# Kernel tuning notes

Hardware: AMD Instinct MI355X
Metric: run time of the kernel (lower is better)

Reference implementation:

```python
import jax, jax.numpy as jnp
import numpy as np

B, QH, QW = 16, 64, 64
KH, KW = 64, 64
H, D, DK, K, S = 8, 256, 32, 4, 1


def setup_inputs() -> dict:
    key = jax.random.key(0)
    ks = jax.random.split(key, 16)
    def lin(i, din, dout, wscale=1.0):
        w = jax.random.normal(ks[i], (din, dout), jnp.float32) * (wscale / np.sqrt(din))
        b = jax.random.normal(ks[i + 1], (dout,), jnp.float32) * 0.02
        return w, b
    Wq, bq = lin(0, D, D)
    Wb, bb = lin(2, D, D)
    Wk, bk = lin(4, D, D)
    Woff, boff = lin(6, D, 2 * H * K * S, wscale=0.1)  # small offsets keep samples near ref point
    WA, bA = lin(8, D, H * K * S)
    Wm, bm = lin(10, D, D)
    return dict(
        query=jax.random.normal(ks[12], (B, QH, QW, D), jnp.float32),
        keys=jax.random.normal(ks[13], (B, KH, KW, D), jnp.float32),
        ref_point=jax.random.uniform(ks[14], (B, QH, QW, 2), jnp.float32),
        src_query=jax.random.normal(ks[15], (B, QH, QW, D), jnp.float32),
        Wq=Wq, bq=bq, Wb=Wb, bb=bb, Wk=Wk, bk=bk,
        Woff=Woff, boff=boff, WA=WA, bA=bA, Wm=Wm, bm=bm)


def _bilinear_zeros(img, px, py):
    # img [N, Hs, Ws, C]; px, py pixel coords [N, K, QH, QW]
    # Matches torch F.grid_sample(mode='bilinear', padding_mode='zeros'):
    # each out-of-bounds corner contributes zero.
    N, Hs, Ws, _ = img.shape
    x0 = jnp.floor(px); y0 = jnp.floor(py)
    wx1 = px - x0; wy1 = py - y0
    n = jnp.arange(N)[:, None, None, None]
    def corner(xf, yf, w):
        xi = xf.astype(jnp.int32); yi = yf.astype(jnp.int32)
        valid = (xi >= 0) & (xi < Ws) & (yi >= 0) & (yi < Hs)
        v = img[n, jnp.clip(yi, 0, Hs - 1), jnp.clip(xi, 0, Ws - 1)]
        return v * (w * valid)[..., None]
    return (corner(x0, y0, (1 - wx1) * (1 - wy1)) + corner(x0 + 1, y0, wx1 * (1 - wy1))
            + corner(x0, y0 + 1, (1 - wx1) * wy1) + corner(x0 + 1, y0 + 1, wx1 * wy1))


def reference(query, keys, ref_point, src_query, Wq, bq, Wb, bb, Wk, bk,
              Woff, boff, WA, bA, Wm, bm):
    _ = query @ Wq + bq  # q_proj output is computed but unused in the original forward
    sq = src_query @ Wb + bb
    off = (sq @ Woff + boff).reshape(B, QH, QW, H, S, K, 2)
    off = off.transpose(0, 3, 4, 5, 1, 2, 6).reshape(B * H, S, K, QH, QW, 2)
    A = jax.nn.softmax((sq @ WA + bA).reshape(B, QH, QW, H, S * K), axis=-1)
    A = A.transpose(0, 3, 1, 2, 4).reshape(B * H, QH, QW, S, K)
    # k_proj on the (single-scale) key feature map -> per-head maps [B*H, KH, KW, DK]
    kf = (keys @ Wk + bk).reshape(B, KH, KW, H, DK).transpose(0, 3, 1, 2, 4).reshape(B * H, KH, KW, DK)
    # restore_scale then torch .repeat(h,1,1,1): flat index n -> batch n % B (faithful to original)
    rr = ref_point * jnp.array([KW - 1, KH - 1], jnp.float32)
    rr = jnp.tile(rr, (H, 1, 1, 1))  # [B*H, QH, QW, 2]
    samples = []
    for l in range(S):
        pts = rr[:, None] + off[:, l]                 # [B*H, K, QH, QW, 2]
        vgx = 2.0 * pts[..., 0] / max(KW - 1, 1) - 1.0
        vgy = 2.0 * pts[..., 1] / max(KH - 1, 1) - 1.0
        px = ((vgx + 1.0) * KW - 1.0) / 2.0           # grid_sample align_corners=False unnormalize
        py = ((vgy + 1.0) * KH - 1.0) / 2.0
        samples.append(_bilinear_zeros(kf, px, py))   # [B*H, K, QH, QW, DK]
    samp = jnp.stack(samples, axis=1)                 # [B*H, S, K, QH, QW, DK]
    feat = jnp.einsum('nskhwd,nhwsk->nhwd', samp, A)  # weighted sum over scales*points
    feat = feat.reshape(B, H, QH, QW, DK).transpose(0, 2, 3, 1, 4).reshape(B, QH, QW, D)
    return feat @ Wm + bm
```

## Files before the change

kernel.cpp:

```cpp
#include <hip/hip_runtime.h>
#include <hip/hip_bf16.h>

using bf16 = __hip_bfloat16;
typedef short bf16x8 __attribute__((ext_vector_type(8)));
typedef float f32x4 __attribute__((ext_vector_type(4)));

#define DD 256
#define MTOT 65536

static __device__ __forceinline__ short f2bs(float f) {
    bf16 h = __float2bfloat16(f);
    return *reinterpret_cast<short*>(&h);
}
static __device__ __forceinline__ float bs2f(short s) {
    unsigned u = (unsigned)(unsigned short)s << 16;
    return __uint_as_float(u);
}

static __device__ __forceinline__ void gll16(const void* g, void* l) {
    __builtin_amdgcn_global_load_lds(
        (const __attribute__((address_space(1))) unsigned int*)g,
        (__attribute__((address_space(3))) unsigned int*)l, 16, 0, 0);
}

static __device__ __forceinline__ int swz_idx(int n, int k) {
    return n * 256 + ((((k >> 3) ^ (n & 7)) << 3) | (k & 7));
}

__global__ __launch_bounds__(256) void k_transpose(
    const float* __restrict__ Wb, const float* __restrict__ Wk, const float* __restrict__ Wm,
    const float* __restrict__ Woff, const float* __restrict__ WA,
    bf16* __restrict__ WbT, bf16* __restrict__ WkT, bf16* __restrict__ WmT,
    bf16* __restrict__ WoffAT)
{
    int idx = blockIdx.x * 256 + threadIdx.x;
    if (idx < 3 * 65536) {
        int which = idx >> 16, e = idx & 65535;
        int i = e >> 8, j = e & 255;
        const float* src = which == 0 ? Wb : (which == 1 ? Wk : Wm);
        bf16*        dst = which == 0 ? WbT : (which == 1 ? WkT : WmT);
        dst[swz_idx(j, i)] = __float2bfloat16(src[e]);
    } else {
        int e = idx - 3 * 65536;
        if (e < 96 * 256) {
            int j = e >> 8, i = e & 255;
            WoffAT[swz_idx(j, i)] = __float2bfloat16((j < 64) ? Woff[i * 64 + j]
                                                              : WA[i * 32 + (j - 64)]);
        }
    }
}

template <int NTW, int NCOLS, bool AF32>
static __device__ __forceinline__ void gemm_lds2(
    const void* __restrict__ Av, const bf16* __restrict__ BTswz,
    bf16* __restrict__ Bs, char* __restrict__ As,
    int row0, int tid, f32x4 (&acc)[2][NTW])
{
    const int wave = tid >> 6, lane = tid & 63;
    const int rg = wave >> 1, cg = wave & 1;
    const int rsub = lane & 15, kg = lane >> 4;
    constexpr int SB = NCOLS / 32;
    constexpr int SA = AF32 ? 4 : 2;
    constexpr int ABYTES = AF32 ? 16384 : 8192;

    auto stageB = [&](int s) {
#pragma unroll
        for (int i = 0; i < SB; ++i) {
            int cc = wave * SB + i;
            int i16 = cc * 64 + lane;
            int n = i16 >> 3, lg = i16 & 7;
            gll16(BTswz + (size_t)n * 256 + s * 64 + lg * 8, (char*)Bs + (size_t)i16 * 16);
        }
    };
    auto stageA = [&](int s, int buf) {
#pragma unroll
        for (int i = 0; i < SA; ++i) {
            if constexpr (AF32) {
                int cc = wave * 4 + i;
                int row = cc * 4 + (lane >> 4);
                int g = (lane & 15) ^ (row & 15);
                gll16((const float*)Av + (size_t)(row0 + row) * DD + s * 64 + g * 4,
                      As + (size_t)buf * ABYTES + cc * 1024 + lane * 16);
            } else {
                int cc = wave * 2 + i;
                int row = cc * 8 + (lane >> 3);
                int g = (lane & 7) ^ (row & 7);
                gll16((const bf16*)Av + (size_t)(row0 + row) * DD + s * 64 + g * 8,
                      As + (size_t)buf * ABYTES + cc * 1024 + lane * 16);
            }
        }
    };

    stageA(0, 0);
    int cur = 0;
#pragma unroll
    for (int s = 0; s < 4; ++s) {
        stageB(s);
        if (s < 3) {
            stageA(s + 1, cur ^ 1);
            asm volatile("s_waitcnt vmcnt(%0)" :: "i"(SA) : "memory");
        } else {
            asm volatile("s_waitcnt vmcnt(0)" ::: "memory");
        }
        __builtin_amdgcn_s_barrier();
#pragma unroll
        for (int kkl = 0; kkl < 2; ++kkl) {
            bf16x8 afr[2];
#pragma unroll
            for (int st = 0; st < 2; ++st) {
                int row = rg * 32 + st * 16 + rsub;
                if constexpr (AF32) {
                    const char* base = As + cur * ABYTES + row * 256;
                    int G0 = kkl * 8 + kg * 2;
                    f32x4 v0 = *(const f32x4*)(base + ((G0 ^ (row & 15)) << 4));
                    f32x4 v1 = *(const f32x4*)(base + (((G0 + 1) ^ (row & 15)) << 4));
                    bf16x8 a;
#pragma unroll
                    for (int e = 0; e < 4; ++e) { a[e] = f2bs(v0[e]); a[e + 4] = f2bs(v1[e]); }
                    afr[st] = a;
                } else {
                    const char* base = As + cur * ABYTES + row * 128;
                    int g = kkl * 4 + kg;
                    afr[st] = *(const bf16x8*)(base + ((g ^ (row & 7)) << 4));
                }
            }
            int lg = kkl * 4 + kg;
#pragma unroll
            for (int nt = 0; nt < NTW; ++nt) {
                int n = cg * (NTW * 16) + nt * 16 + rsub;
                bf16x8 b = *(const bf16x8*)((const char*)Bs + (size_t)n * 128 + ((lg ^ (n & 7)) << 4));
                acc[0][nt] = __builtin_amdgcn_mfma_f32_16x16x32_bf16(afr[0], b, acc[0][nt], 0, 0, 0);
                acc[1][nt] = __builtin_amdgcn_mfma_f32_16x16x32_bf16(afr[1], b, acc[1][nt], 0, 0, 0);
            }
        }
        asm volatile("s_waitcnt lgkmcnt(0)" ::: "memory");
        __builtin_amdgcn_s_barrier();
        cur ^= 1;
    }
}

__global__ __launch_bounds__(256) void k_gemm_sq(
    const float* __restrict__ src, const bf16* __restrict__ WbT,
    const float* __restrict__ bb, bf16* __restrict__ sq)
{
    __shared__ __align__(16) bf16 Bs[256 * 64];
    __shared__ __align__(16) char As[2 * 16384];
    int tid = threadIdx.x, lane = tid & 63, wave = tid >> 6;
    int row0 = blockIdx.x * 64;
    f32x4 acc[2][8] = {};
    gemm_lds2<8, 256, true>(src, WbT, Bs, As, row0, tid, acc);
    int col = lane & 15;
    int jbase = (wave & 1) * 128;
    int rb = row0 + (wave >> 1) * 32 + ((lane >> 4) << 2);
#pragma unroll
    for (int mt = 0; mt < 2; ++mt)
#pragma unroll
        for (int nt = 0; nt < 8; ++nt) {
            int j = jbase + nt * 16 + col;
            float bias = bb[j];
#pragma unroll
            for (int r = 0; r < 4; ++r)
                sq[(size_t)(rb + mt * 16 + r) * DD + j] =
                    __float2bfloat16(acc[mt][nt][r] + bias);
        }
}

__global__ __launch_bounds__(256) void k_gemm_offA(
    const bf16* __restrict__ sq, const bf16* __restrict__ WoffAT,
    const float* __restrict__ boff, const float* __restrict__ bA,
    float* __restrict__ off_ws, float* __restrict__ A_ws)
{
    __shared__ __align__(16) bf16 Bs[96 * 64];
    __shared__ __align__(16) char As[2 * 8192];
    int tid = threadIdx.x, lane = tid & 63, wave = tid >> 6;
    int row0 = blockIdx.x * 64;
    f32x4 acc[2][3] = {};
    gemm_lds2<3, 96, false>(sq, WoffAT, Bs, As, row0, tid, acc);
    int col = lane & 15;
    int jbase = (wave & 1) * 48;
    int rb = row0 + (wave >> 1) * 32 + ((lane >> 4) << 2);
#pragma unroll
    for (int mt = 0; mt < 2; ++mt) {
#pragma unroll
        for (int nt = 0; nt < 3; ++nt) {
            int j = jbase + nt * 16 + col;
            if (j < 64) {
                float bias = boff[j];
#pragma unroll
                for (int r = 0; r < 4; ++r) {
                    int m = rb + mt * 16 + r;
                    off_ws[(size_t)m * 64 + j] = acc[mt][nt][r] + bias;
                }
            } else {
                int ac = j - 64;
                float bias = bA[ac];
#pragma unroll
                for (int r = 0; r < 4; ++r) {
                    int m = rb + mt * 16 + r;
                    float v  = acc[mt][nt][r] + bias;
                    float mx = fmaxf(v, __shfl_xor(v, 1));
                    mx       = fmaxf(mx, __shfl_xor(mx, 2));
                    float e  = __expf(v - mx);
                    float su = e + __shfl_xor(e, 1);
                    su      += __shfl_xor(su, 2);
                    A_ws[(size_t)m * 32 + ac] = e / su;
                }
            }
        }
    }
}

__global__ __launch_bounds__(256) void k_gemm_kf(
    const float* __restrict__ keys, const bf16* __restrict__ WkT,
    const float* __restrict__ bk, bf16* __restrict__ kf)
{
    __shared__ __align__(16) bf16 Bs[256 * 64];
    __shared__ __align__(16) char As[2 * 16384];
    int tid = threadIdx.x, lane = tid & 63, wave = tid >> 6;
    int row0 = blockIdx.x * 64;
    f32x4 acc[2][8] = {};
    gemm_lds2<8, 256, true>(keys, WkT, Bs, As, row0, tid, acc);
    int col = lane & 15;
    int jbase = (wave & 1) * 128;
    int rb = row0 + (wave >> 1) * 32 + ((lane >> 4) << 2);
#pragma unroll
    for (int mt = 0; mt < 2; ++mt)
#pragma unroll
        for (int nt = 0; nt < 8; ++nt) {
            int j = jbase + nt * 16 + col;
            float bias = bk[j];
#pragma unroll
            for (int r = 0; r < 4; ++r) {
                int m = rb + mt * 16 + r;
                size_t dst = (((size_t)(m >> 12) * 8 + (j >> 5)) * 4096 + (m & 4095)) * 32 + (j & 31);
                kf[dst] = __float2bfloat16(acc[mt][nt][r] + bias);
            }
        }
}

__global__ __launch_bounds__(256) void k_sample(
    const float* __restrict__ ref_point, const float* __restrict__ off_ws,
    const float* __restrict__ A_ws, const bf16* __restrict__ kf,
    bf16* __restrict__ feat)
{
    int t  = threadIdx.x;
    int q  = t >> 5;
    int h  = (t >> 2) & 7;
    int cg = t & 3;
    int m  = blockIdx.x * 8 + q;
    int b  = m >> 12, pix = m & 4095;
    int rbatch = (b * 8 + h) & 15;
    const float* rp = ref_point + ((size_t)rbatch * 4096 + pix) * 2;
    float rx = rp[0] * 63.0f;
    float ry = rp[1] * 63.0f;
    const bf16* kfh = kf + ((size_t)(b * 8 + h) * 4096) * 32 + cg * 8;
    float acc[8] = {};
#pragma unroll
    for (int k = 0; k < 4; ++k) {
        const float* op = off_ws + (size_t)m * 64 + (h * 4 + k) * 2;
        float ox = op[0], oy = op[1];
        float a  = A_ws[(size_t)m * 32 + h * 4 + k];
        float px = (rx + ox) * (64.0f / 63.0f) - 0.5f;
        float py = (ry + oy) * (64.0f / 63.0f) - 0.5f;
        float x0 = floorf(px), y0 = floorf(py);
        float wx1 = px - x0, wy1 = py - y0;
        int xi = (int)x0, yi = (int)y0;
        float ax0 = (1.f - wx1) * ((xi     >= 0 && xi     < 64) ? 1.f : 0.f);
        float ax1 = wx1         * ((xi + 1 >= 0 && xi + 1 < 64) ? 1.f : 0.f);
        float ay0 = (1.f - wy1) * ((yi     >= 0 && yi     < 64) ? a : 0.f);
        float ay1 = wy1         * ((yi + 1 >= 0 && yi + 1 < 64) ? a : 0.f);
        int xc0 = min(max(xi, 0), 63),      xc1 = min(max(xi + 1, 0), 63);
        int yc0 = min(max(yi, 0), 63) * 64, yc1 = min(max(yi + 1, 0), 63) * 64;
        bf16x8 v00 = *(const bf16x8*)(kfh + (yc0 + xc0) * 32);
        bf16x8 v01 = *(const bf16x8*)(kfh + (yc0 + xc1) * 32);
        bf16x8 v10 = *(const bf16x8*)(kfh + (yc1 + xc0) * 32);
        bf16x8 v11 = *(const bf16x8*)(kfh + (yc1 + xc1) * 32);
        float w00 = ax0 * ay0, w01 = ax1 * ay0, w10 = ax0 * ay1, w11 = ax1 * ay1;
#pragma unroll
        for (int e = 0; e < 8; ++e) {
            acc[e] += w00 * bs2f(v00[e]) + w01 * bs2f(v01[e])
                    + w10 * bs2f(v10[e]) + w11 * bs2f(v11[e]);
        }
    }
    bf16x8 o;
#pragma unroll
    for (int e = 0; e < 8; ++e) o[e] = f2bs(acc[e]);
    *(bf16x8*)(feat + (size_t)m * DD + h * 32 + cg * 8) = o;
}

__global__ __launch_bounds__(256) void k_gemm_out(
    const bf16* __restrict__ feat, const bf16* __restrict__ WmT,
    const float* __restrict__ bm, float* __restrict__ out)
{
    __shared__ __align__(16) bf16 Bs[256 * 64];
    __shared__ __align__(16) char As[2 * 8192];
    int tid = threadIdx.x, lane = tid & 63, wave = tid >> 6;
    int row0 = blockIdx.x * 64;
    f32x4 acc[2][8] = {};
    gemm_lds2<8, 256, false>(feat, WmT, Bs, As, row0, tid, acc);
    int col = lane & 15;
    int jbase = (wave & 1) * 128;
    int rb = row0 + (wave >> 1) * 32 + ((lane >> 4) << 2);
#pragma unroll
    for (int mt = 0; mt < 2; ++mt)
#pragma unroll
        for (int nt = 0; nt < 8; ++nt) {
            int j = jbase + nt * 16 + col;
            float bias = bm[j];
#pragma unroll
            for (int r = 0; r < 4; ++r)
                out[(size_t)(rb + mt * 16 + r) * DD + j] =
                    acc[mt][nt][r] + bias;
        }
}

extern "C" void kernel_launch(void* const* d_in, const int* in_sizes, int n_in,
                              void* d_out, int out_size, void* d_ws, size_t ws_size,
                              hipStream_t stream)
{
    (void)in_sizes; (void)n_in; (void)out_size; (void)ws_size;
    const float* keys = (const float*)d_in[1];
    const float* refp = (const float*)d_in[2];
    const float* srcq = (const float*)d_in[3];
    const float* Wb   = (const float*)d_in[6];
    const float* bb   = (const float*)d_in[7];
    const float* Wk   = (const float*)d_in[8];
    const float* bk   = (const float*)d_in[9];
    const float* Woff = (const float*)d_in[10];
    const float* boff = (const float*)d_in[11];
    const float* WA   = (const float*)d_in[12];
    const float* bA   = (const float*)d_in[13];
    const float* Wm   = (const float*)d_in[14];
    const float* bm   = (const float*)d_in[15];

    char* ws = (char*)d_ws;
    bf16*  WbT    = (bf16*)(ws + 0);
    bf16*  WkT    = (bf16*)(ws + 131072);
    bf16*  WmT    = (bf16*)(ws + 262144);
    bf16*  WoffAT = (bf16*)(ws + 393216);
    bf16*  sq_ws  = (bf16*)(ws + 442368);
    bf16*  kf_ws  = (bf16*)(ws + 442368 + 33554432ull);
    bf16*  feat_ws= (bf16*)(ws + 442368 + 2ull * 33554432ull);
    float* off_ws = (float*)(ws + 442368 + 3ull * 33554432ull);
    float* A_ws   = (float*)(ws + 442368 + 3ull * 33554432ull + 16777216ull);

    float* out = (float*)d_out;

    k_transpose<<<864, 256, 0, stream>>>(Wb, Wk, Wm, Woff, WA, WbT, WkT, WmT, WoffAT);
    k_gemm_sq  <<<1024, 256, 0, stream>>>(srcq, WbT, bb, sq_ws);
    k_gemm_kf  <<<1024, 256, 0, stream>>>(keys, WkT, bk, kf_ws);
    k_gemm_offA<<<1024, 256, 0, stream>>>(sq_ws, WoffAT, boff, bA, off_ws, A_ws);
    k_sample   <<<8192, 256, 0, stream>>>(refp, off_ws, A_ws, kf_ws, feat_ws);
    k_gemm_out <<<1024, 256, 0, stream>>>(feat_ws, WmT, bm, out);
}
```

Before: 134.7 us.

## Fuse sq projection with offset/attention GEMM via LDS and remap sample blocks by XCD

```diff
diff --git a/kernel.cpp b/kernel.cpp
--- a/kernel.cpp
+++ b/kernel.cpp
@@ -139,9 +139,10 @@
     }
 }
 
-__global__ __launch_bounds__(256) void k_gemm_sq(
-    const float* __restrict__ src, const bf16* __restrict__ WbT,
-    const float* __restrict__ bb, bf16* __restrict__ sq)
+__global__ __launch_bounds__(256) void k_gemm_sqoffA(
+    const float* __restrict__ src, const bf16* __restrict__ WbT, const float* __restrict__ bb,
+    const bf16* __restrict__ WoffAT, const float* __restrict__ boff, const float* __restrict__ bA,
+    float* __restrict__ off_ws, float* __restrict__ A_ws)
 {
     __shared__ __align__(16) bf16 Bs[256 * 64];
     __shared__ __align__(16) char As[2 * 16384];
@@ -149,36 +150,77 @@
     int row0 = blockIdx.x * 64;
     f32x4 acc[2][8] = {};
     gemm_lds2<8, 256, true>(src, WbT, Bs, As, row0, tid, acc);
+
+    {
+        int col = lane & 15;
+        int jbase = (wave & 1) * 128;
+        int lrb = (wave >> 1) * 32 + ((lane >> 4) << 2);
+#pragma unroll
+        for (int mt = 0; mt < 2; ++mt)
+#pragma unroll
+            for (int nt = 0; nt < 8; ++nt) {
+                int j = jbase + nt * 16 + col;
+                float bias = bb[j];
+                int g = j >> 3;
+#pragma unroll
+                for (int r = 0; r < 4; ++r) {
+                    int lr = lrb + mt * 16 + r;
+                    *(short*)(As + lr * 512 + (((g ^ (lr & 7)) << 4)) + (j & 7) * 2) =
+                        f2bs(acc[mt][nt][r] + bias);
+                }
+            }
+    }
+    __syncthreads();
+
+    f32x4 acc2[2][3] = {};
+    const int rsub = lane & 15, kg = lane >> 4;
+    const int rg = wave >> 1, cg2 = wave & 1;
+    auto stageOB = [&](int s, int buf) {
+#pragma unroll
+        for (int i = 0; i < 3; ++i) {
+            int i16 = (wave * 3 + i) * 64 + lane;
+            int n = i16 >> 3, lg = i16 & 7;
+            gll16(WoffAT + (size_t)n * 256 + s * 64 + lg * 8,
+                  (char*)Bs + buf * 12288 + (size_t)i16 * 16);
+        }
+    };
+    stageOB(0, 0);
+    int cur = 0;
+#pragma unroll
+    for (int s = 0; s < 4; ++s) {
+        if (s < 3) {
+            stageOB(s + 1, cur ^ 1);
+            asm volatile("s_waitcnt vmcnt(3)" ::: "memory");
+        } else {
+            asm volatile("s_waitcnt vmcnt(0)" ::: "memory");
+        }
+        __builtin_amdgcn_s_barrier();
+#pragma unroll
+        for (int kkl = 0; kkl < 2; ++kkl) {
+            bf16x8 afr[2];
+#pragma unroll
+            for (int st = 0; st < 2; ++st) {
+                int lr = rg * 32 + st * 16 + rsub;
+                int g = s * 8 + kkl * 4 + kg;
+                afr[st] = *(const bf16x8*)(As + lr * 512 + ((g ^ (lr & 7)) << 4));
+            }
+            int lg = kkl * 4 + kg;
+#pragma unroll
+            for (int nt = 0; nt < 3; ++nt) {
+                int n = cg2 * 48 + nt * 16 + rsub;
+                bf16x8 b = *(const bf16x8*)((const char*)Bs + cur * 12288 + (size_t)n * 128
+                                            + ((lg ^ (n & 7)) << 4));
+                acc2[0][nt] = __builtin_amdgcn_mfma_f32_16x16x32_bf16(afr[0], b, acc2[0][nt], 0, 0, 0);
+                acc2[1][nt] = __builtin_amdgcn_mfma_f32_16x16x32_bf16(afr[1], b, acc2[1][nt], 0, 0, 0);
+            }
+        }
+        asm volatile("s_waitcnt lgkmcnt(0)" ::: "memory");
+        __builtin_amdgcn_s_barrier();
+        cur ^= 1;
+    }
     int col = lane & 15;
-    int jbase = (wave & 1) * 128;
-    int rb = row0 + (wave >> 1) * 32 + ((lane >> 4) << 2);
-#pragma unroll
-    for (int mt = 0; mt < 2; ++mt)
-#pragma unroll
-        for (int nt = 0; nt < 8; ++nt) {
-            int j = jbase + nt * 16 + col;
-            float bias = bb[j];
-#pragma unroll
-            for (int r = 0; r < 4; ++r)
-                sq[(size_t)(rb + mt * 16 + r) * DD + j] =
-                    __float2bfloat16(acc[mt][nt][r] + bias);
-        }
-}
-
-__global__ __launch_bounds__(256) void k_gemm_offA(
-    const bf16* __restrict__ sq, const bf16* __restrict__ WoffAT,
-    const float* __restrict__ boff, const float* __restrict__ bA,
-    float* __restrict__ off_ws, float* __restrict__ A_ws)
-{
-    __shared__ __align__(16) bf16 Bs[96 * 64];
-    __shared__ __align__(16) char As[2 * 8192];
-    int tid = threadIdx.x, lane = tid & 63, wave = tid >> 6;
-    int row0 = blockIdx.x * 64;
-    f32x4 acc[2][3] = {};
-    gemm_lds2<3, 96, false>(sq, WoffAT, Bs, As, row0, tid, acc);
-    int col = lane & 15;
-    int jbase = (wave & 1) * 48;
-    int rb = row0 + (wave >> 1) * 32 + ((lane >> 4) << 2);
+    int jbase = cg2 * 48;
+    int rb = row0 + rg * 32 + ((lane >> 4) << 2);
 #pragma unroll
     for (int mt = 0; mt < 2; ++mt) {
 #pragma unroll
@@ -189,7 +231,7 @@
 #pragma unroll
                 for (int r = 0; r < 4; ++r) {
                     int m = rb + mt * 16 + r;
-                    off_ws[(size_t)m * 64 + j] = acc[mt][nt][r] + bias;
+                    off_ws[(size_t)m * 64 + j] = acc2[mt][nt][r] + bias;
                 }
             } else {
                 int ac = j - 64;
@@ -197,7 +239,7 @@
 #pragma unroll
                 for (int r = 0; r < 4; ++r) {
                     int m = rb + mt * 16 + r;
-                    float v  = acc[mt][nt][r] + bias;
+                    float v  = acc2[mt][nt][r] + bias;
                     float mx = fmaxf(v, __shfl_xor(v, 1));
                     mx       = fmaxf(mx, __shfl_xor(mx, 2));
                     float e  = __expf(v - mx);
@@ -243,12 +285,16 @@
     const float* __restrict__ A_ws, const bf16* __restrict__ kf,
     bf16* __restrict__ feat)
 {
+    int bid = blockIdx.x;
+    int xcd = bid & 7, within = bid >> 3;
+    int bb_ = xcd * 2 + (within >> 9);
+    int pixblk = within & 511;
     int t  = threadIdx.x;
     int q  = t >> 5;
     int h  = (t >> 2) & 7;
     int cg = t & 3;
-    int m  = blockIdx.x * 8 + q;
-    int b  = m >> 12, pix = m & 4095;
+    int m  = (bb_ << 12) + pixblk * 8 + q;
+    int b  = bb_, pix = m & 4095;
     int rbatch = (b * 8 + h) & 15;
     const float* rp = ref_point + ((size_t)rbatch * 4096 + pix) * 2;
     float rx = rp[0] * 63.0f;
@@ -338,7 +384,6 @@
     bf16*  WkT    = (bf16*)(ws + 131072);
     bf16*  WmT    = (bf16*)(ws + 262144);
     bf16*  WoffAT = (bf16*)(ws + 393216);
-    bf16*  sq_ws  = (bf16*)(ws + 442368);
     bf16*  kf_ws  = (bf16*)(ws + 442368 + 33554432ull);
     bf16*  feat_ws= (bf16*)(ws + 442368 + 2ull * 33554432ull);
     float* off_ws = (float*)(ws + 442368 + 3ull * 33554432ull);
@@ -346,10 +391,9 @@
 
     float* out = (float*)d_out;
 
-    k_transpose<<<864, 256, 0, stream>>>(Wb, Wk, Wm, Woff, WA, WbT, WkT, WmT, WoffAT);
-    k_gemm_sq  <<<1024, 256, 0, stream>>>(srcq, WbT, bb, sq_ws);
-    k_gemm_kf  <<<1024, 256, 0, stream>>>(keys, WkT, bk, kf_ws);
-    k_gemm_offA<<<1024, 256, 0, stream>>>(sq_ws, WoffAT, boff, bA, off_ws, A_ws);
-    k_sample   <<<8192, 256, 0, stream>>>(refp, off_ws, A_ws, kf_ws, feat_ws);
-    k_gemm_out <<<1024, 256, 0, stream>>>(feat_ws, WmT, bm, out);
-}
+    k_transpose  <<<864, 256, 0, stream>>>(Wb, Wk, Wm, Woff, WA, WbT, WkT, WmT, WoffAT);
+    k_gemm_sqoffA<<<1024, 256, 0, stream>>>(srcq, WbT, bb, WoffAT, boff, bA, off_ws, A_ws);
+    k_gemm_kf    <<<1024, 256, 0, stream>>>(keys, WkT, bk, kf_ws);
+    k_sample     <<<8192, 256, 0, stream>>>(refp, off_ws, A_ws, kf_ws, feat_ws);
+    k_gemm_out   <<<1024, 256, 0, stream>>>(feat_ws, WmT, bm, out);
+}
```

Measured after the change: 122.6 us. 1.1x faster.

## Fold Wb projection into offset/attention weights, remove sq GEMM

Applied to the files above, without the earlier changes.

```diff
diff --git a/kernel.cpp b/kernel.cpp
--- a/kernel.cpp
+++ b/kernel.cpp
@@ -28,26 +28,39 @@
 }
 
 __global__ __launch_bounds__(256) void k_transpose(
-    const float* __restrict__ Wb, const float* __restrict__ Wk, const float* __restrict__ Wm,
-    const float* __restrict__ Woff, const float* __restrict__ WA,
-    bf16* __restrict__ WbT, bf16* __restrict__ WkT, bf16* __restrict__ WmT,
-    bf16* __restrict__ WoffAT)
+    const float* __restrict__ Wk, const float* __restrict__ Wm,
+    bf16* __restrict__ WkT, bf16* __restrict__ WmT)
 {
     int idx = blockIdx.x * 256 + threadIdx.x;
-    if (idx < 3 * 65536) {
-        int which = idx >> 16, e = idx & 65535;
-        int i = e >> 8, j = e & 255;
-        const float* src = which == 0 ? Wb : (which == 1 ? Wk : Wm);
-        bf16*        dst = which == 0 ? WbT : (which == 1 ? WkT : WmT);
-        dst[swz_idx(j, i)] = __float2bfloat16(src[e]);
-    } else {
-        int e = idx - 3 * 65536;
-        if (e < 96 * 256) {
-            int j = e >> 8, i = e & 255;
-            WoffAT[swz_idx(j, i)] = __float2bfloat16((j < 64) ? Woff[i * 64 + j]
-                                                              : WA[i * 32 + (j - 64)]);
-        }
+    int which = idx >> 16, e = idx & 65535;
+    int i = e >> 8, j = e & 255;
+    const float* src = which == 0 ? Wk : Wm;
+    bf16*        dst = which == 0 ? WkT : WmT;
+    dst[swz_idx(j, i)] = __float2bfloat16(src[e]);
+}
+
+__global__ __launch_bounds__(256) void k_prep(
+    const float* __restrict__ Wb, const float* __restrict__ bb,
+    const float* __restrict__ Woff, const float* __restrict__ boff,
+    const float* __restrict__ WA, const float* __restrict__ bA,
+    bf16* __restrict__ WCt, float* __restrict__ bc)
+{
+    __shared__ float colw[256];
+    __shared__ float red[256];
+    int j = blockIdx.x, t = threadIdx.x;
+    colw[t] = (j < 64) ? Woff[t * 64 + j] : WA[t * 32 + (j - 64)];
+    red[t] = bb[t] * ((j < 64) ? Woff[t * 64 + j] : WA[t * 32 + (j - 64)]);
+    __syncthreads();
+    float v = 0.f;
+    const float* wbrow = Wb + (size_t)t * 256;
+#pragma unroll 8
+    for (int i = 0; i < 256; ++i) v += wbrow[i] * colw[i];
+    WCt[swz_idx(j, t)] = __float2bfloat16(v);
+    for (int s = 128; s > 0; s >>= 1) {
+        __syncthreads();
+        if (t < s) red[t] += red[t + s];
     }
+    if (t == 0) bc[j] = red[0] + ((j < 64) ? boff[j] : bA[j - 64]);
 }
 
 template <int NTW, int NCOLS, bool AF32>
@@ -139,43 +152,16 @@
     }
 }
 
-__global__ __launch_bounds__(256) void k_gemm_sq(
-    const float* __restrict__ src, const bf16* __restrict__ WbT,
-    const float* __restrict__ bb, bf16* __restrict__ sq)
-{
-    __shared__ __align__(16) bf16 Bs[256 * 64];
+__global__ __launch_bounds__(256) void k_offA(
+    const float* __restrict__ src, const bf16* __restrict__ WCt, const float* __restrict__ bc,
+    float* __restrict__ off_ws, float* __restrict__ A_ws)
+{
+    __shared__ __align__(16) bf16 Bs[96 * 64];
     __shared__ __align__(16) char As[2 * 16384];
     int tid = threadIdx.x, lane = tid & 63, wave = tid >> 6;
     int row0 = blockIdx.x * 64;
-    f32x4 acc[2][8] = {};
-    gemm_lds2<8, 256, true>(src, WbT, Bs, As, row0, tid, acc);
-    int col = lane & 15;
-    int jbase = (wave & 1) * 128;
-    int rb = row0 + (wave >> 1) * 32 + ((lane >> 4) << 2);
-#pragma unroll
-    for (int mt = 0; mt < 2; ++mt)
-#pragma unroll
-        for (int nt = 0; nt < 8; ++nt) {
-            int j = jbase + nt * 16 + col;
-            float bias = bb[j];
-#pragma unroll
-            for (int r = 0; r < 4; ++r)
-                sq[(size_t)(rb + mt * 16 + r) * DD + j] =
-                    __float2bfloat16(acc[mt][nt][r] + bias);
-        }
-}
-
-__global__ __launch_bounds__(256) void k_gemm_offA(
-    const bf16* __restrict__ sq, const bf16* __restrict__ WoffAT,
-    const float* __restrict__ boff, const float* __restrict__ bA,
-    float* __restrict__ off_ws, float* __restrict__ A_ws)
-{
-    __shared__ __align__(16) bf16 Bs[96 * 64];
-    __shared__ __align__(16) char As[2 * 8192];
-    int tid = threadIdx.x, lane = tid & 63, wave = tid >> 6;
-    int row0 = blockIdx.x * 64;
     f32x4 acc[2][3] = {};
-    gemm_lds2<3, 96, false>(sq, WoffAT, Bs, As, row0, tid, acc);
+    gemm_lds2<3, 96, true>(src, WCt, Bs, As, row0, tid, acc);
     int col = lane & 15;
     int jbase = (wave & 1) * 48;
     int rb = row0 + (wave >> 1) * 32 + ((lane >> 4) << 2);
@@ -185,7 +171,7 @@
         for (int nt = 0; nt < 3; ++nt) {
             int j = jbase + nt * 16 + col;
             if (j < 64) {
-                float bias = boff[j];
+                float bias = bc[j];
 #pragma unroll
                 for (int r = 0; r < 4; ++r) {
                     int m = rb + mt * 16 + r;
@@ -193,7 +179,7 @@
                 }
             } else {
                 int ac = j - 64;
-                float bias = bA[ac];
+                float bias = bc[j];
 #pragma unroll
                 for (int r = 0; r < 4; ++r) {
                     int m = rb + mt * 16 + r;
@@ -243,23 +229,30 @@
     const float* __restrict__ A_ws, const bf16* __restrict__ kf,
     bf16* __restrict__ feat)
 {
+    int bid = blockIdx.x;
+    int xcd = bid & 7, within = bid >> 3;
+    int bb_ = xcd * 2 + (within >> 9);
+    int pixblk = within & 511;
     int t  = threadIdx.x;
     int q  = t >> 5;
     int h  = (t >> 2) & 7;
     int cg = t & 3;
-    int m  = blockIdx.x * 8 + q;
-    int b  = m >> 12, pix = m & 4095;
+    int m  = (bb_ << 12) + pixblk * 8 + q;
+    int b  = bb_, pix = m & 4095;
     int rbatch = (b * 8 + h) & 15;
     const float* rp = ref_point + ((size_t)rbatch * 4096 + pix) * 2;
     float rx = rp[0] * 63.0f;
     float ry = rp[1] * 63.0f;
     const bf16* kfh = kf + ((size_t)(b * 8 + h) * 4096) * 32 + cg * 8;
+    f32x4 o0 = *(const f32x4*)(off_ws + (size_t)m * 64 + h * 8);
+    f32x4 o1 = *(const f32x4*)(off_ws + (size_t)m * 64 + h * 8 + 4);
+    f32x4 av = *(const f32x4*)(A_ws  + (size_t)m * 32 + h * 4);
     float acc[8] = {};
 #pragma unroll
     for (int k = 0; k < 4; ++k) {
-        const float* op = off_ws + (size_t)m * 64 + (h * 4 + k) * 2;
-        float ox = op[0], oy = op[1];
-        float a  = A_ws[(size_t)m * 32 + h * 4 + k];
+        float ox = (k < 2) ? o0[2 * k] : o1[2 * k - 4];
+        float oy = (k < 2) ? o0[2 * k + 1] : o1[2 * k - 3];
+        float a  = av[k];
         float px = (rx + ox) * (64.0f / 63.0f) - 0.5f;
         float py = (ry + oy) * (64.0f / 63.0f) - 0.5f;
         float x0 = floorf(px), y0 = floorf(py);
@@ -334,11 +327,10 @@
     const float* bm   = (const float*)d_in[15];
 
     char* ws = (char*)d_ws;
-    bf16*  WbT    = (bf16*)(ws + 0);
-    bf16*  WkT    = (bf16*)(ws + 131072);
-    bf16*  WmT    = (bf16*)(ws + 262144);
-    bf16*  WoffAT = (bf16*)(ws + 393216);
-    bf16*  sq_ws  = (bf16*)(ws + 442368);
+    bf16*  WkT    = (bf16*)(ws + 0);
+    bf16*  WmT    = (bf16*)(ws + 131072);
+    bf16*  WCt    = (bf16*)(ws + 262144);
+    float* bc     = (float*)(ws + 311296);
     bf16*  kf_ws  = (bf16*)(ws + 442368 + 33554432ull);
     bf16*  feat_ws= (bf16*)(ws + 442368 + 2ull * 33554432ull);
     float* off_ws = (float*)(ws + 442368 + 3ull * 33554432ull);
@@ -346,10 +338,10 @@
 
     float* out = (float*)d_out;
 
-    k_transpose<<<864, 256, 0, stream>>>(Wb, Wk, Wm, Woff, WA, WbT, WkT, WmT, WoffAT);
-    k_gemm_sq  <<<1024, 256, 0, stream>>>(srcq, WbT, bb, sq_ws);
+    k_transpose<<<512, 256, 0, stream>>>(Wk, Wm, WkT, WmT);
+    k_prep     <<<96, 256, 0, stream>>>(Wb, bb, Woff, boff, WA, bA, WCt, bc);
+    k_offA     <<<1024, 256, 0, stream>>>(srcq, WCt, bc, off_ws, A_ws);
     k_gemm_kf  <<<1024, 256, 0, stream>>>(keys, WkT, bk, kf_ws);
-    k_gemm_offA<<<1024, 256, 0, stream>>>(sq_ws, WoffAT, boff, bA, off_ws, A_ws);
     k_sample   <<<8192, 256, 0, stream>>>(refp, off_ws, A_ws, kf_ws, feat_ws);
     k_gemm_out <<<1024, 256, 0, stream>>>(feat_ws, WmT, bm, out);
 }
```

After: 122.1 us. 9.4% less time.
